# Kernel optimization log

Measured on AMD Instinct MI355X. Metric: run time of the kernel, lower is better.

## Reference

```python
import jax, jax.numpy as jnp
import numpy as np

HEAD_NUM = 8
QKV_DIM = 16
SQRT_EMBEDDING_DIM = 11.313708498984761  # sqrt(128)
LOGIT_CLIPPING = 10.0


def _reshape_by_heads(x):
    # x: [B, n, H*D] -> [B, H, n, D]
    B, n, _ = x.shape
    return x.reshape(B, n, HEAD_NUM, QKV_DIM).transpose(0, 2, 1, 3)


def setup_inputs() -> dict:
    key = jax.random.key(0)
    ks = jax.random.split(key, 12)
    B, P, N, E = 64, 500, 501, 128
    HD = HEAD_NUM * QKV_DIM
    s = 0.05
    return {
        "encoded_last_node": jax.random.normal(ks[0], (B, P, E), jnp.float32),
        "load": jax.random.uniform(ks[1], (B, P), jnp.float32),
        "ninf_mask": jnp.zeros((B, P, N), jnp.float32),
        "encoded_nodes": jax.random.normal(ks[2], (B, N, E), jnp.float32),
        "Wq_last": jax.random.normal(ks[3], (E + 1, HD), jnp.float32) * s,
        "Wk": jax.random.normal(ks[4], (E, HD), jnp.float32) * s,
        "Wv": jax.random.normal(ks[5], (E, HD), jnp.float32) * s,
        "mhc_W": jax.random.normal(ks[6], (HD, E), jnp.float32) * s,
        "mhc_b": jax.random.normal(ks[7], (E,), jnp.float32) * s,
        "new": jax.random.normal(ks[8], (B, HD, HD), jnp.float32) * s,
        "new_bias": jax.random.normal(ks[9], (B, 1, HD), jnp.float32) * s,
        "new_2": jax.random.normal(ks[10], (B, HD, HD), jnp.float32) * s,
        "new_bias_2": jax.random.normal(ks[11], (B, 1, HD), jnp.float32) * s,
    }


def reference(encoded_last_node, load, ninf_mask, encoded_nodes,
              Wq_last, Wk, Wv, mhc_W, mhc_b,
              new, new_bias, new_2, new_bias_2):
    B, P, E = encoded_last_node.shape
    # set_kv
    k = _reshape_by_heads(encoded_nodes @ Wk)            # [B,H,N,D]
    v = _reshape_by_heads(encoded_nodes @ Wv)            # [B,H,N,D]
    single_head_key = encoded_nodes.transpose(0, 2, 1)   # [B,E,N]

    # q from (last node embedding, load)
    input_cat = jnp.concatenate([encoded_last_node, load[:, :, None]], axis=2)  # [B,P,E+1]
    q = _reshape_by_heads(input_cat @ Wq_last)           # [B,H,P,D]

    # multi-head attention
    score = jnp.einsum('bhpd,bhnd->bhpn', q, k) / jnp.sqrt(jnp.float32(QKV_DIM))
    score = score + ninf_mask[:, None, :, :]
    attn = jax.nn.softmax(score, axis=3)
    out = jnp.einsum('bhpn,bhnd->bhpd', attn, v)         # [B,H,P,D]
    out_concat = out.transpose(0, 2, 1, 3).reshape(B, P, HEAD_NUM * QKV_DIM)

    # per-batch affine + relu + residual
    residual = out_concat
    h = jax.nn.relu(jnp.matmul(out_concat, new) + new_bias)
    h = jnp.matmul(h, new_2) + new_bias_2 + residual

    mh_atten_out = h @ mhc_W + mhc_b                     # [B,P,E]

    score2 = jnp.matmul(mh_atten_out, single_head_key)   # [B,P,N]
    score_clipped = LOGIT_CLIPPING * jnp.tanh(score2 / SQRT_EMBEDDING_DIM)
    probs = jax.nn.softmax(score_clipped + ninf_mask, axis=2)
    return probs
```

## Files before the change

### kernel.cpp

```cpp
#include <hip/hip_runtime.h>
#include <hip/hip_bf16.h>
#include <math.h>

typedef float f4 __attribute__((ext_vector_type(4)));

#define FMA __builtin_fmaf

#define BATCH 64
#define PP 500
#define NN 501

__global__ __launch_bounds__(256) void k_proj(
    const float* __restrict__ Xq,
    const float* __restrict__ Ld,
    const float* __restrict__ Xn,
    const float* __restrict__ Wq,
    const float* __restrict__ Wk, const float* __restrict__ Wv,
    float* __restrict__ Q, float* __restrict__ K_, float* __restrict__ V_)
{
  __shared__ float xs[64*132];
  const int t = threadIdx.x;
  const int tr = t >> 5, tc = t & 31;
  if (blockIdx.x < 500) {
    const int r0 = blockIdx.x * 64;
    for (int i = t; i < 64*32; i += 256) {
      int r = i >> 5, k4 = (i & 31) << 2;
      *(f4*)(xs + r*132 + k4) = *(const f4*)(Xq + (size_t)(r0+r)*128 + k4);
    }
    if (t < 64) xs[t*132 + 128] = Ld[r0 + t];
    __syncthreads();
    float acc[8][4];
    #pragma unroll
    for (int i = 0; i < 8; i++)
      #pragma unroll
      for (int c = 0; c < 4; c++) acc[i][c] = 0.f;
    for (int k4 = 0; k4 < 128; k4 += 4) {
      f4 x[8], w[4];
      #pragma unroll
      for (int j = 0; j < 4; j++) w[j] = *(const f4*)(Wq + (size_t)(k4+j)*128 + tc*4);
      #pragma unroll
      for (int i = 0; i < 8; i++) x[i] = *(const f4*)(xs + (tr*8+i)*132 + k4);
      #pragma unroll
      for (int i = 0; i < 8; i++)
        #pragma unroll
        for (int j = 0; j < 4; j++)
          #pragma unroll
          for (int c = 0; c < 4; c++)
            acc[i][c] = FMA(x[i][j], w[j][c], acc[i][c]);
    }
    {
      f4 w = *(const f4*)(Wq + (size_t)128*128 + tc*4);
      #pragma unroll
      for (int i = 0; i < 8; i++) {
        float xv = xs[(tr*8+i)*132 + 128];
        #pragma unroll
        for (int c = 0; c < 4; c++) acc[i][c] = FMA(xv, w[c], acc[i][c]);
      }
    }
    #pragma unroll
    for (int i = 0; i < 8; i++) {
      f4 o;
      #pragma unroll
      for (int c = 0; c < 4; c++) o[c] = acc[i][c];
      *(f4*)(Q + (size_t)(r0 + tr*8 + i)*128 + tc*4) = o;
    }
  } else {
    const int r0 = (blockIdx.x - 500) * 64;
    for (int i = t; i < 64*32; i += 256) {
      int r = i >> 5, k4 = (i & 31) << 2;
      *(f4*)(xs + r*132 + k4) = *(const f4*)(Xn + (size_t)(r0+r)*128 + k4);
    }
    __syncthreads();
    float accK[8][4], accV[8][4];
    #pragma unroll
    for (int i = 0; i < 8; i++)
      #pragma unroll
      for (int c = 0; c < 4; c++) { accK[i][c] = 0.f; accV[i][c] = 0.f; }
    for (int k4 = 0; k4 < 128; k4 += 4) {
      f4 x[8], wk[4], wv[4];
      #pragma unroll
      for (int j = 0; j < 4; j++) {
        wk[j] = *(const f4*)(Wk + (size_t)(k4+j)*128 + tc*4);
        wv[j] = *(const f4*)(Wv + (size_t)(k4+j)*128 + tc*4);
      }
      #pragma unroll
      for (int i = 0; i < 8; i++) x[i] = *(const f4*)(xs + (tr*8+i)*132 + k4);
      #pragma unroll
      for (int i = 0; i < 8; i++)
        #pragma unroll
        for (int j = 0; j < 4; j++)
          #pragma unroll
          for (int c = 0; c < 4; c++) {
            accK[i][c] = FMA(x[i][j], wk[j][c], accK[i][c]);
            accV[i][c] = FMA(x[i][j], wv[j][c], accV[i][c]);
          }
    }
    #pragma unroll
    for (int i = 0; i < 8; i++) {
      f4 ok, ov;
      #pragma unroll
      for (int c = 0; c < 4; c++) { ok[c] = accK[i][c]; ov[c] = accV[i][c]; }
      *(f4*)(K_ + (size_t)(r0 + tr*8 + i)*128 + tc*4) = ok;
      *(f4*)(V_ + (size_t)(r0 + tr*8 + i)*128 + tc*4) = ov;
    }
  }
}

__global__ __launch_bounds__(256, 4) void k_attn(
    const float* __restrict__ Q, const float* __restrict__ K_, const float* __restrict__ V_,
    const float* __restrict__ Msk, float* __restrict__ OC)
{
  __shared__ float ks[32*132];
  __shared__ float vs[32*132];
  __shared__ float mks[32*33];
  const int blk = blockIdx.x;
  const int b  = blk >> 4;
  const int pt = blk & 15;
  const int p0 = pt * 32;
  const int t = threadIdx.x;
  const int h   = t >> 5;
  const int row = t & 31;
  const bool pvalid = (p0 + row) < PP;
  const int p = pvalid ? (p0 + row) : (PP - 1);

  f4 q0, q1, q2, q3;
  {
    const float* qrow = Q + ((size_t)b*PP + p)*128 + h*16;
    q0 = *(const f4*)(qrow);
    q1 = *(const f4*)(qrow + 4);
    q2 = *(const f4*)(qrow + 8);
    q3 = *(const f4*)(qrow + 12);
  }

  const int mr = t >> 3, nq = (t & 7) << 2;
  const int grow = min(p0 + mr, PP - 1);
  const float* gm = Msk + ((size_t)b*PP + grow)*NN;

  float m_r = -1e30f, l_r = 0.f;
  f4 o0 = {0.f,0.f,0.f,0.f}, o1 = o0, o2 = o0, o3 = o0;

  f4 kpre[4], vpre[4]; float mk[4];
  #pragma unroll
  for (int u = 0; u < 4; u++) {
    int i = t + u*256;
    int n = i >> 5, d4 = (i & 31) << 2;
    kpre[u] = *(const f4*)(K_ + ((size_t)b*NN + n)*128 + d4);
    vpre[u] = *(const f4*)(V_ + ((size_t)b*NN + n)*128 + d4);
  }
  #pragma unroll
  for (int j = 0; j < 4; j++)
    mk[j] = (nq + j < NN) ? gm[nq + j] : -1e30f;

  for (int c0 = 0; c0 < NN; c0 += 32) {
    #pragma unroll
    for (int u = 0; u < 4; u++) {
      int i = t + u*256;
      int n = i >> 5, d4 = (i & 31) << 2;
      *(f4*)(ks + n*132 + d4) = kpre[u];
      *(f4*)(vs + n*132 + d4) = vpre[u];
    }
    {
      float* dm = mks + mr*33 + nq;
      #pragma unroll
      for (int j = 0; j < 4; j++) dm[j] = mk[j];
    }
    __syncthreads();

    const int c1 = c0 + 32;
    if (c1 < NN) {
      #pragma unroll
      for (int u = 0; u < 4; u++) {
        int i = t + u*256;
        int n = i >> 5, d4 = (i & 31) << 2;
        int ng = c1 + n;
        f4 kv = {0.f,0.f,0.f,0.f}, vv = {0.f,0.f,0.f,0.f};
        if (ng < NN) {
          kv = *(const f4*)(K_ + ((size_t)b*NN + ng)*128 + d4);
          vv = *(const f4*)(V_ + ((size_t)b*NN + ng)*128 + d4);
        }
        kpre[u] = kv; vpre[u] = vv;
      }
      #pragma unroll
      for (int j = 0; j < 4; j++)
        mk[j] = (c1 + nq + j < NN) ? gm[c1 + nq + j] : -1e30f;
    }

    const float* ksh = ks + h*16;
    const float* vsh = vs + h*16;
    const float* mrw = mks + row*33;
    #pragma unroll
    for (int n = 0; n < 32; n++) {
      const float* kf = ksh + n*132;
      f4 k0 = *(const f4*)(kf);
      f4 k1 = *(const f4*)(kf + 4);
      f4 k2 = *(const f4*)(kf + 8);
      f4 k3 = *(const f4*)(kf + 12);
      float s = 0.f;
      #pragma unroll
      for (int d = 0; d < 4; d++) s = FMA(q0[d], k0[d], s);
      #pragma unroll
      for (int d = 0; d < 4; d++) s = FMA(q1[d], k1[d], s);
      #pragma unroll
      for (int d = 0; d < 4; d++) s = FMA(q2[d], k2[d], s);
      #pragma unroll
      for (int d = 0; d < 4; d++) s = FMA(q3[d], k3[d], s);
      s = FMA(s, 0.25f, mrw[n]);
      if (s > m_r) {
        float cc = __expf(m_r - s);
        m_r = s;
        l_r *= cc;
        o0 *= cc; o1 *= cc; o2 *= cc; o3 *= cc;
      }
      float e = __expf(s - m_r);
      l_r += e;
      const float* vf = vsh + n*132;
      f4 v0 = *(const f4*)(vf);
      f4 v1 = *(const f4*)(vf + 4);
      f4 v2 = *(const f4*)(vf + 8);
      f4 v3 = *(const f4*)(vf + 12);
      #pragma unroll
      for (int d = 0; d < 4; d++) {
        o0[d] = FMA(e, v0[d], o0[d]);
        o1[d] = FMA(e, v1[d], o1[d]);
        o2[d] = FMA(e, v2[d], o2[d]);
        o3[d] = FMA(e, v3[d], o3[d]);
      }
    }
    __syncthreads();
  }

  if (pvalid) {
    float inv = 1.f / l_r;
    float* orow = OC + ((size_t)b*PP + p)*128 + h*16;
    *(f4*)(orow)      = o0 * inv;
    *(f4*)(orow + 4)  = o1 * inv;
    *(f4*)(orow + 8)  = o2 * inv;
    *(f4*)(orow + 12) = o3 * inv;
  }
}

__global__ __launch_bounds__(256) void k_ffn(
    const float* __restrict__ OC, const float* __restrict__ Wn, const float* __restrict__ Bn,
    const float* __restrict__ Wn2, const float* __restrict__ Bn2,
    const float* __restrict__ Wm, const float* __restrict__ Bm,
    float* __restrict__ MH)
{
  __shared__ float xs[64*132];
  __shared__ float hs[64*132];
  const int blk = blockIdx.x; const int b = blk >> 3, rb = blk & 7;
  const int r0 = rb*64;
  const int nv = min(64, PP - r0);
  const int t = threadIdx.x;
  const int tr = t >> 5, tc = t & 31;
  const float* ocb = OC + (size_t)b*PP*128;
  for (int i = t; i < 64*32; i += 256) {
    int r = i >> 5, k4 = (i & 31) << 2;
    f4 v = {0.f,0.f,0.f,0.f};
    if (r < nv) v = *(const f4*)(ocb + (size_t)(r0+r)*128 + k4);
    *(f4*)(xs + r*132 + k4) = v;
  }
  __syncthreads();
  {
    const float* W1 = Wn + (size_t)b*16384;
    float acc[8][4];
    #pragma unroll
    for (int i = 0; i < 8; i++)
      #pragma unroll
      for (int c = 0; c < 4; c++) acc[i][c] = 0.f;
    for (int k4 = 0; k4 < 128; k4 += 4) {
      f4 x[8], w[4];
      #pragma unroll
      for (int j = 0; j < 4; j++) w[j] = *(const f4*)(W1 + (size_t)(k4+j)*128 + tc*4);
      #pragma unroll
      for (int i = 0; i < 8; i++) x[i] = *(const f4*)(xs + (tr*8+i)*132 + k4);
      #pragma unroll
      for (int i = 0; i < 8; i++)
        #pragma unroll
        for (int j = 0; j < 4; j++)
          #pragma unroll
          for (int c = 0; c < 4; c++)
            acc[i][c] = FMA(x[i][j], w[j][c], acc[i][c]);
    }
    f4 b1 = *(const f4*)(Bn + b*128 + tc*4);
    #pragma unroll
    for (int i = 0; i < 8; i++) {
      f4 o;
      #pragma unroll
      for (int c = 0; c < 4; c++) o[c] = fmaxf(acc[i][c] + b1[c], 0.f);
      *(f4*)(hs + (tr*8+i)*132 + tc*4) = o;
    }
  }
  __syncthreads();
  float h2[8][4];
  {
    const float* W2 = Wn2 + (size_t)b*16384;
    float acc[8][4];
    #pragma unroll
    for (int i = 0; i < 8; i++)
      #pragma unroll
      for (int c = 0; c < 4; c++) acc[i][c] = 0.f;
    for (int k4 = 0; k4 < 128; k4 += 4) {
      f4 x[8], w[4];
      #pragma unroll
      for (int j = 0; j < 4; j++) w[j] = *(const f4*)(W2 + (size_t)(k4+j)*128 + tc*4);
      #pragma unroll
      for (int i = 0; i < 8; i++) x[i] = *(const f4*)(hs + (tr*8+i)*132 + k4);
      #pragma unroll
      for (int i = 0; i < 8; i++)
        #pragma unroll
        for (int j = 0; j < 4; j++)
          #pragma unroll
          for (int c = 0; c < 4; c++)
            acc[i][c] = FMA(x[i][j], w[j][c], acc[i][c]);
    }
    f4 b2 = *(const f4*)(Bn2 + b*128 + tc*4);
    #pragma unroll
    for (int i = 0; i < 8; i++)
      #pragma unroll
      for (int c = 0; c < 4; c++)
        h2[i][c] = acc[i][c] + b2[c] + xs[(tr*8+i)*132 + tc*4 + c];
  }
  __syncthreads();
  #pragma unroll
  for (int i = 0; i < 8; i++) {
    f4 o;
    #pragma unroll
    for (int c = 0; c < 4; c++) o[c] = h2[i][c];
    *(f4*)(hs + (tr*8+i)*132 + tc*4) = o;
  }
  __syncthreads();
  {
    float acc[8][4];
    #pragma unroll
    for (int i = 0; i < 8; i++)
      #pragma unroll
      for (int c = 0; c < 4; c++) acc[i][c] = 0.f;
    for (int k4 = 0; k4 < 128; k4 += 4) {
      f4 x[8], w[4];
      #pragma unroll
      for (int j = 0; j < 4; j++) w[j] = *(const f4*)(Wm + (size_t)(k4+j)*128 + tc*4);
      #pragma unroll
      for (int i = 0; i < 8; i++) x[i] = *(const f4*)(hs + (tr*8+i)*132 + k4);
      #pragma unroll
      for (int i = 0; i < 8; i++)
        #pragma unroll
        for (int j = 0; j < 4; j++)
          #pragma unroll
          for (int c = 0; c < 4; c++)
            acc[i][c] = FMA(x[i][j], w[j][c], acc[i][c]);
    }
    f4 b3 = *(const f4*)(Bm + tc*4);
    #pragma unroll
    for (int i = 0; i < 8; i++) {
      if (tr*8 + i < nv) {
        f4 o;
        #pragma unroll
        for (int c = 0; c < 4; c++) o[c] = acc[i][c] + b3[c];
        *(f4*)(MH + ((size_t)b*PP + r0 + tr*8 + i)*128 + tc*4) = o;
      }
    }
  }
}

__global__ __launch_bounds__(256, 3) void k_final(
    const float* __restrict__ MH, const float* __restrict__ EN,
    const float* __restrict__ Msk, float* __restrict__ OUT)
{
  __shared__ float ms[32*132];
  __shared__ float es[64*132];
  const int blk = blockIdx.x; const int b = blk >> 4, rb = blk & 15;
  const int r0 = rb*32; const int nv = min(32, PP - r0);
  const int t = threadIdx.x;
  const int tr = t >> 5, tc = t & 31;
  const float* mhb = MH + (size_t)(b*PP + r0)*128;
  for (int i = t; i < 32*32; i += 256) {
    int r = i >> 5, k4 = (i & 31) << 2;
    f4 v = {0.f,0.f,0.f,0.f};
    if (r < nv) v = *(const f4*)(mhb + (size_t)r*128 + k4);
    *(f4*)(ms + r*132 + k4) = v;
  }
  const float* enb = EN + (size_t)b*NN*128;
  f4 epre[8];
  #pragma unroll
  for (int u = 0; u < 8; u++) {
    int i = t + u*256;
    int n = i >> 5, k4 = (i & 31) << 2;
    f4 v = {0.f,0.f,0.f,0.f};
    if (n < NN) v = *(const f4*)(enb + (size_t)n*128 + k4);
    epre[u] = v;
  }
  float s[8][4][2];
  #pragma unroll
  for (int nt = 0; nt < 8; nt++) {
    #pragma unroll
    for (int u = 0; u < 8; u++) {
      int i = t + u*256;
      int n = i >> 5, k4 = (i & 31) << 2;
      *(f4*)(es + n*132 + k4) = epre[u];
    }
    __syncthreads();
    if (nt < 7) {
      const int n1 = (nt+1)*64;
      #pragma unroll
      for (int u = 0; u < 8; u++) {
        int i = t + u*256;
        int n = i >> 5, k4 = (i & 31) << 2;
        f4 v = {0.f,0.f,0.f,0.f};
        if (n1 + n < NN) v = *(const f4*)(enb + (size_t)(n1+n)*128 + k4);
        epre[u] = v;
      }
    }
    float acc[4][2];
    #pragma unroll
    for (int i = 0; i < 4; i++) { acc[i][0] = 0.f; acc[i][1] = 0.f; }
    #pragma unroll 8
    for (int k4 = 0; k4 < 128; k4 += 4) {
      f4 x[4];
      #pragma unroll
      for (int i = 0; i < 4; i++) x[i] = *(const f4*)(ms + (tr*4+i)*132 + k4);
      f4 e0 = *(const f4*)(es + tc*132 + k4);
      f4 e1 = *(const f4*)(es + (tc+32)*132 + k4);
      #pragma unroll
      for (int i = 0; i < 4; i++)
        #pragma unroll
        for (int j = 0; j < 4; j++) {
          acc[i][0] = FMA(x[i][j], e0[j], acc[i][0]);
          acc[i][1] = FMA(x[i][j], e1[j], acc[i][1]);
        }
    }
    #pragma unroll
    for (int i = 0; i < 4; i++) {
      s[nt][i][0] = acc[i][0];
      s[nt][i][1] = acc[i][1];
    }
    __syncthreads();
  }
  const float* mkb = Msk + (size_t)(b*PP + r0)*NN;
  #pragma unroll
  for (int nt = 0; nt < 8; nt++)
    #pragma unroll
    for (int i = 0; i < 4; i++)
      #pragma unroll
      for (int c = 0; c < 2; c++) {
        int r = tr*4 + i, n = nt*64 + tc + c*32;
        float val = -INFINITY;
        if (r < nv && n < NN) {
          float E = __expf(s[nt][i][c] * 0.17677669529663687f);
          val = 10.f - 20.f/(E + 1.f) + mkb[(size_t)r*NN + n];
        }
        s[nt][i][c] = val;
      }
  float* ob = OUT + (size_t)(b*PP + r0)*NN;
  #pragma unroll
  for (int i = 0; i < 4; i++) {
    float m = -INFINITY;
    #pragma unroll
    for (int nt = 0; nt < 8; nt++)
      #pragma unroll
      for (int c = 0; c < 2; c++) m = fmaxf(m, s[nt][i][c]);
    #pragma unroll
    for (int o = 16; o > 0; o >>= 1) m = fmaxf(m, __shfl_xor(m, o, 32));
    float l = 0.f;
    #pragma unroll
    for (int nt = 0; nt < 8; nt++)
      #pragma unroll
      for (int c = 0; c < 2; c++) {
        float e_ = __expf(s[nt][i][c] - m);
        s[nt][i][c] = e_;
        l += e_;
      }
    #pragma unroll
    for (int o = 16; o > 0; o >>= 1) l += __shfl_xor(l, o, 32);
    const int r = tr*4 + i;
    if (r < nv) {
      float inv = 1.f / l;
      float* orow = ob + (size_t)r*NN;
      #pragma unroll
      for (int nt = 0; nt < 8; nt++)
        #pragma unroll
        for (int c = 0; c < 2; c++) {
          int n = nt*64 + tc + c*32;
          if (n < NN) orow[n] = s[nt][i][c] * inv;
        }
    }
  }
}

extern "C" void kernel_launch(void* const* d_in, const int* in_sizes, int n_in,
                              void* d_out, int out_size, void* d_ws, size_t ws_size,
                              hipStream_t stream) {
  const float* eln  = (const float*)d_in[0];
  const float* load = (const float*)d_in[1];
  const float* mask = (const float*)d_in[2];
  const float* en   = (const float*)d_in[3];
  const float* Wq   = (const float*)d_in[4];
  const float* Wk   = (const float*)d_in[5];
  const float* Wv   = (const float*)d_in[6];
  const float* Wm   = (const float*)d_in[7];
  const float* Bm   = (const float*)d_in[8];
  const float* Wn   = (const float*)d_in[9];
  const float* Bn   = (const float*)d_in[10];
  const float* Wn2  = (const float*)d_in[11];
  const float* Bn2  = (const float*)d_in[12];
  float* out = (float*)d_out;
  float* ws  = (float*)d_ws;
  float* Q   = ws;
  float* K_  = ws + 4096000;
  float* V_  = ws + 8200192;
  float* OC  = ws + 12304384;
  float* MH  = ws + 16400384;
  hipLaunchKernelGGL(k_proj,  dim3(1001), dim3(256), 0, stream, eln, load, en, Wq, Wk, Wv, Q, K_, V_);
  hipLaunchKernelGGL(k_attn,  dim3(1024), dim3(256), 0, stream, Q, K_, V_, mask, OC);
  hipLaunchKernelGGL(k_ffn,   dim3(512),  dim3(256), 0, stream, OC, Wn, Bn, Wn2, Bn2, Wm, Bm, MH);
  hipLaunchKernelGGL(k_final, dim3(1024), dim3(256), 0, stream, MH, en, mask, out);
}
```

Measured before the change: 406.2 us.

## Fuse attention, FFN, projection and final softmax into one kernel

Merges k_attn, k_ffn and k_final into a single kernel that works on a 32-row tile per block. The attention output, the FFN intermediates and the mh output stay in shared memory instead of making round trips through global workspace, and two kernel launches go away. In exchange, the FFN tile shrinks from 64 to 32 rows, so per-batch weights are reloaded twice as often. The final score loop now uses 32-column tiles with a 16x4 register array. Occupancy is lowered to 3 blocks per SM, and the serial chain inside each block gets longer.

```diff
diff --git a/kernel.cpp b/kernel.cpp
--- a/kernel.cpp
+++ b/kernel.cpp
@@ -11,10 +11,8 @@
 #define NN 501
 
 __global__ __launch_bounds__(256) void k_proj(
-    const float* __restrict__ Xq,
-    const float* __restrict__ Ld,
-    const float* __restrict__ Xn,
-    const float* __restrict__ Wq,
+    const float* __restrict__ Xq, const float* __restrict__ Ld,
+    const float* __restrict__ Xn, const float* __restrict__ Wq,
     const float* __restrict__ Wk, const float* __restrict__ Wv,
     float* __restrict__ Q, float* __restrict__ K_, float* __restrict__ V_)
 {
@@ -106,382 +104,338 @@
   }
 }
 
-__global__ __launch_bounds__(256, 4) void k_attn(
+__global__ __launch_bounds__(256, 3) void k_fused(
     const float* __restrict__ Q, const float* __restrict__ K_, const float* __restrict__ V_,
-    const float* __restrict__ Msk, float* __restrict__ OC)
+    const float* __restrict__ Msk, const float* __restrict__ EN,
+    const float* __restrict__ Wn, const float* __restrict__ Bn,
+    const float* __restrict__ Wn2, const float* __restrict__ Bn2,
+    const float* __restrict__ Wm, const float* __restrict__ Bm,
+    float* __restrict__ OUT)
 {
-  __shared__ float ks[32*132];
-  __shared__ float vs[32*132];
+  __shared__ float sA[32*132];
+  __shared__ float sB[32*132];
   __shared__ float mks[32*33];
   const int blk = blockIdx.x;
   const int b  = blk >> 4;
   const int pt = blk & 15;
   const int p0 = pt * 32;
+  const int nv = min(32, PP - p0);
   const int t = threadIdx.x;
-  const int h   = t >> 5;
-  const int row = t & 31;
-  const bool pvalid = (p0 + row) < PP;
-  const int p = pvalid ? (p0 + row) : (PP - 1);
-
-  f4 q0, q1, q2, q3;
+
   {
-    const float* qrow = Q + ((size_t)b*PP + p)*128 + h*16;
-    q0 = *(const f4*)(qrow);
-    q1 = *(const f4*)(qrow + 4);
-    q2 = *(const f4*)(qrow + 8);
-    q3 = *(const f4*)(qrow + 12);
-  }
-
-  const int mr = t >> 3, nq = (t & 7) << 2;
-  const int grow = min(p0 + mr, PP - 1);
-  const float* gm = Msk + ((size_t)b*PP + grow)*NN;
-
-  float m_r = -1e30f, l_r = 0.f;
-  f4 o0 = {0.f,0.f,0.f,0.f}, o1 = o0, o2 = o0, o3 = o0;
-
-  f4 kpre[4], vpre[4]; float mk[4];
-  #pragma unroll
-  for (int u = 0; u < 4; u++) {
-    int i = t + u*256;
-    int n = i >> 5, d4 = (i & 31) << 2;
-    kpre[u] = *(const f4*)(K_ + ((size_t)b*NN + n)*128 + d4);
-    vpre[u] = *(const f4*)(V_ + ((size_t)b*NN + n)*128 + d4);
-  }
-  #pragma unroll
-  for (int j = 0; j < 4; j++)
-    mk[j] = (nq + j < NN) ? gm[nq + j] : -1e30f;
-
-  for (int c0 = 0; c0 < NN; c0 += 32) {
+    const int h   = t >> 5;
+    const int row = t & 31;
+    const bool pvalid = (p0 + row) < PP;
+    const int p = pvalid ? (p0 + row) : (PP - 1);
+
+    f4 q0, q1, q2, q3;
+    {
+      const float* qrow = Q + ((size_t)b*PP + p)*128 + h*16;
+      q0 = *(const f4*)(qrow);
+      q1 = *(const f4*)(qrow + 4);
+      q2 = *(const f4*)(qrow + 8);
+      q3 = *(const f4*)(qrow + 12);
+    }
+    const int mr = t >> 3, nq = (t & 7) << 2;
+    const int grow = min(p0 + mr, PP - 1);
+    const float* gm = Msk + ((size_t)b*PP + grow)*NN;
+
+    float m_r = -1e30f, l_r = 0.f;
+    f4 o0 = {0.f,0.f,0.f,0.f}, o1 = o0, o2 = o0, o3 = o0;
+
+    f4 kpre[4], vpre[4]; float mk[4];
     #pragma unroll
     for (int u = 0; u < 4; u++) {
       int i = t + u*256;
       int n = i >> 5, d4 = (i & 31) << 2;
-      *(f4*)(ks + n*132 + d4) = kpre[u];
-      *(f4*)(vs + n*132 + d4) = vpre[u];
-    }
-    {
-      float* dm = mks + mr*33 + nq;
-      #pragma unroll
-      for (int j = 0; j < 4; j++) dm[j] = mk[j];
-    }
-    __syncthreads();
-
-    const int c1 = c0 + 32;
-    if (c1 < NN) {
+      kpre[u] = *(const f4*)(K_ + ((size_t)b*NN + n)*128 + d4);
+      vpre[u] = *(const f4*)(V_ + ((size_t)b*NN + n)*128 + d4);
+    }
+    #pragma unroll
+    for (int j = 0; j < 4; j++)
+      mk[j] = (nq + j < NN) ? gm[nq + j] : -1e30f;
+
+    for (int c0 = 0; c0 < NN; c0 += 32) {
       #pragma unroll
       for (int u = 0; u < 4; u++) {
         int i = t + u*256;
         int n = i >> 5, d4 = (i & 31) << 2;
-        int ng = c1 + n;
-        f4 kv = {0.f,0.f,0.f,0.f}, vv = {0.f,0.f,0.f,0.f};
-        if (ng < NN) {
-          kv = *(const f4*)(K_ + ((size_t)b*NN + ng)*128 + d4);
-          vv = *(const f4*)(V_ + ((size_t)b*NN + ng)*128 + d4);
-        }
-        kpre[u] = kv; vpre[u] = vv;
-      }
-      #pragma unroll
-      for (int j = 0; j < 4; j++)
-        mk[j] = (c1 + nq + j < NN) ? gm[c1 + nq + j] : -1e30f;
-    }
-
-    const float* ksh = ks + h*16;
-    const float* vsh = vs + h*16;
-    const float* mrw = mks + row*33;
-    #pragma unroll
-    for (int n = 0; n < 32; n++) {
-      const float* kf = ksh + n*132;
-      f4 k0 = *(const f4*)(kf);
-      f4 k1 = *(const f4*)(kf + 4);
-      f4 k2 = *(const f4*)(kf + 8);
-      f4 k3 = *(const f4*)(kf + 12);
-      float s = 0.f;
-      #pragma unroll
-      for (int d = 0; d < 4; d++) s = FMA(q0[d], k0[d], s);
-      #pragma unroll
-      for (int d = 0; d < 4; d++) s = FMA(q1[d], k1[d], s);
-      #pragma unroll
-      for (int d = 0; d < 4; d++) s = FMA(q2[d], k2[d], s);
-      #pragma unroll
-      for (int d = 0; d < 4; d++) s = FMA(q3[d], k3[d], s);
-      s = FMA(s, 0.25f, mrw[n]);
-      if (s > m_r) {
-        float cc = __expf(m_r - s);
-        m_r = s;
-        l_r *= cc;
-        o0 *= cc; o1 *= cc; o2 *= cc; o3 *= cc;
-      }
-      float e = __expf(s - m_r);
-      l_r += e;
-      const float* vf = vsh + n*132;
-      f4 v0 = *(const f4*)(vf);
-      f4 v1 = *(const f4*)(vf + 4);
-      f4 v2 = *(const f4*)(vf + 8);
-      f4 v3 = *(const f4*)(vf + 12);
-      #pragma unroll
-      for (int d = 0; d < 4; d++) {
-        o0[d] = FMA(e, v0[d], o0[d]);
-        o1[d] = FMA(e, v1[d], o1[d]);
-        o2[d] = FMA(e, v2[d], o2[d]);
-        o3[d] = FMA(e, v3[d], o3[d]);
-      }
-    }
-    __syncthreads();
-  }
-
-  if (pvalid) {
+        *(f4*)(sA + n*132 + d4) = kpre[u];
+        *(f4*)(sB + n*132 + d4) = vpre[u];
+      }
+      {
+        float* dm = mks + mr*33 + nq;
+        #pragma unroll
+        for (int j = 0; j < 4; j++) dm[j] = mk[j];
+      }
+      __syncthreads();
+
+      const int c1 = c0 + 32;
+      if (c1 < NN) {
+        #pragma unroll
+        for (int u = 0; u < 4; u++) {
+          int i = t + u*256;
+          int n = i >> 5, d4 = (i & 31) << 2;
+          int ng = c1 + n;
+          f4 kv = {0.f,0.f,0.f,0.f}, vv = {0.f,0.f,0.f,0.f};
+          if (ng < NN) {
+            kv = *(const f4*)(K_ + ((size_t)b*NN + ng)*128 + d4);
+            vv = *(const f4*)(V_ + ((size_t)b*NN + ng)*128 + d4);
+          }
+          kpre[u] = kv; vpre[u] = vv;
+        }
+        #pragma unroll
+        for (int j = 0; j < 4; j++)
+          mk[j] = (c1 + nq + j < NN) ? gm[c1 + nq + j] : -1e30f;
+      }
+
+      const float* ksh = sA + h*16;
+      const float* vsh = sB + h*16;
+      const float* mrw = mks + row*33;
+      #pragma unroll
+      for (int n = 0; n < 32; n++) {
+        const float* kf = ksh + n*132;
+        f4 k0 = *(const f4*)(kf);
+        f4 k1 = *(const f4*)(kf + 4);
+        f4 k2 = *(const f4*)(kf + 8);
+        f4 k3 = *(const f4*)(kf + 12);
+        float s = 0.f;
+        #pragma unroll
+        for (int d = 0; d < 4; d++) s = FMA(q0[d], k0[d], s);
+        #pragma unroll
+        for (int d = 0; d < 4; d++) s = FMA(q1[d], k1[d], s);
+        #pragma unroll
+        for (int d = 0; d < 4; d++) s = FMA(q2[d], k2[d], s);
+        #pragma unroll
+        for (int d = 0; d < 4; d++) s = FMA(q3[d], k3[d], s);
+        s = FMA(s, 0.25f, mrw[n]);
+        if (s > m_r) {
+          float cc = __expf(m_r - s);
+          m_r = s;
+          l_r *= cc;
+          o0 *= cc; o1 *= cc; o2 *= cc; o3 *= cc;
+        }
+        float e = __expf(s - m_r);
+        l_r += e;
+        const float* vf = vsh + n*132;
+        f4 v0 = *(const f4*)(vf);
+        f4 v1 = *(const f4*)(vf + 4);
+        f4 v2 = *(const f4*)(vf + 8);
+        f4 v3 = *(const f4*)(vf + 12);
+        #pragma unroll
+        for (int d = 0; d < 4; d++) {
+          o0[d] = FMA(e, v0[d], o0[d]);
+          o1[d] = FMA(e, v1[d], o1[d]);
+          o2[d] = FMA(e, v2[d], o2[d]);
+          o3[d] = FMA(e, v3[d], o3[d]);
+        }
+      }
+      __syncthreads();
+    }
+
     float inv = 1.f / l_r;
-    float* orow = OC + ((size_t)b*PP + p)*128 + h*16;
-    *(f4*)(orow)      = o0 * inv;
-    *(f4*)(orow + 4)  = o1 * inv;
-    *(f4*)(orow + 8)  = o2 * inv;
-    *(f4*)(orow + 12) = o3 * inv;
-  }
-}
-
-__global__ __launch_bounds__(256) void k_ffn(
-    const float* __restrict__ OC, const float* __restrict__ Wn, const float* __restrict__ Bn,
-    const float* __restrict__ Wn2, const float* __restrict__ Bn2,
-    const float* __restrict__ Wm, const float* __restrict__ Bm,
-    float* __restrict__ MH)
-{
-  __shared__ float xs[64*132];
-  __shared__ float hs[64*132];
-  const int blk = blockIdx.x; const int b = blk >> 3, rb = blk & 7;
-  const int r0 = rb*64;
-  const int nv = min(64, PP - r0);
-  const int t = threadIdx.x;
-  const int tr = t >> 5, tc = t & 31;
-  const float* ocb = OC + (size_t)b*PP*128;
-  for (int i = t; i < 64*32; i += 256) {
-    int r = i >> 5, k4 = (i & 31) << 2;
-    f4 v = {0.f,0.f,0.f,0.f};
-    if (r < nv) v = *(const f4*)(ocb + (size_t)(r0+r)*128 + k4);
-    *(f4*)(xs + r*132 + k4) = v;
+    float* xr = sA + row*132 + h*16;
+    *(f4*)(xr)      = o0 * inv;
+    *(f4*)(xr + 4)  = o1 * inv;
+    *(f4*)(xr + 8)  = o2 * inv;
+    *(f4*)(xr + 12) = o3 * inv;
   }
   __syncthreads();
+
+  const int tr = t >> 5, tc = t & 31;
   {
-    const float* W1 = Wn + (size_t)b*16384;
-    float acc[8][4];
-    #pragma unroll
-    for (int i = 0; i < 8; i++)
-      #pragma unroll
-      for (int c = 0; c < 4; c++) acc[i][c] = 0.f;
-    for (int k4 = 0; k4 < 128; k4 += 4) {
-      f4 x[8], w[4];
-      #pragma unroll
-      for (int j = 0; j < 4; j++) w[j] = *(const f4*)(W1 + (size_t)(k4+j)*128 + tc*4);
-      #pragma unroll
-      for (int i = 0; i < 8; i++) x[i] = *(const f4*)(xs + (tr*8+i)*132 + k4);
-      #pragma unroll
-      for (int i = 0; i < 8; i++)
-        #pragma unroll
-        for (int j = 0; j < 4; j++)
-          #pragma unroll
-          for (int c = 0; c < 4; c++)
-            acc[i][c] = FMA(x[i][j], w[j][c], acc[i][c]);
-    }
-    f4 b1 = *(const f4*)(Bn + b*128 + tc*4);
-    #pragma unroll
-    for (int i = 0; i < 8; i++) {
+    {
+      const float* W1 = Wn + (size_t)b*16384;
+      float acc[4][4];
+      #pragma unroll
+      for (int i = 0; i < 4; i++)
+        #pragma unroll
+        for (int c = 0; c < 4; c++) acc[i][c] = 0.f;
+      for (int k4 = 0; k4 < 128; k4 += 4) {
+        f4 x[4], w[4];
+        #pragma unroll
+        for (int j = 0; j < 4; j++) w[j] = *(const f4*)(W1 + (size_t)(k4+j)*128 + tc*4);
+        #pragma unroll
+        for (int i = 0; i < 4; i++) x[i] = *(const f4*)(sA + (tr*4+i)*132 + k4);
+        #pragma unroll
+        for (int i = 0; i < 4; i++)
+          #pragma unroll
+          for (int j = 0; j < 4; j++)
+            #pragma unroll
+            for (int c = 0; c < 4; c++)
+              acc[i][c] = FMA(x[i][j], w[j][c], acc[i][c]);
+      }
+      f4 b1 = *(const f4*)(Bn + b*128 + tc*4);
+      #pragma unroll
+      for (int i = 0; i < 4; i++) {
+        f4 o;
+        #pragma unroll
+        for (int c = 0; c < 4; c++) o[c] = fmaxf(acc[i][c] + b1[c], 0.f);
+        *(f4*)(sB + (tr*4+i)*132 + tc*4) = o;
+      }
+    }
+    __syncthreads();
+    float h2[4][4];
+    {
+      const float* W2 = Wn2 + (size_t)b*16384;
+      float acc[4][4];
+      #pragma unroll
+      for (int i = 0; i < 4; i++)
+        #pragma unroll
+        for (int c = 0; c < 4; c++) acc[i][c] = 0.f;
+      for (int k4 = 0; k4 < 128; k4 += 4) {
+        f4 x[4], w[4];
+        #pragma unroll
+        for (int j = 0; j < 4; j++) w[j] = *(const f4*)(W2 + (size_t)(k4+j)*128 + tc*4);
+        #pragma unroll
+        for (int i = 0; i < 4; i++) x[i] = *(const f4*)(sB + (tr*4+i)*132 + k4);
+        #pragma unroll
+        for (int i = 0; i < 4; i++)
+          #pragma unroll
+          for (int j = 0; j < 4; j++)
+            #pragma unroll
+            for (int c = 0; c < 4; c++)
+              acc[i][c] = FMA(x[i][j], w[j][c], acc[i][c]);
+      }
+      f4 b2 = *(const f4*)(Bn2 + b*128 + tc*4);
+      #pragma unroll
+      for (int i = 0; i < 4; i++)
+        #pragma unroll
+        for (int c = 0; c < 4; c++)
+          h2[i][c] = acc[i][c] + b2[c] + sA[(tr*4+i)*132 + tc*4 + c];
+    }
+    __syncthreads();
+    #pragma unroll
+    for (int i = 0; i < 4; i++) {
       f4 o;
       #pragma unroll
-      for (int c = 0; c < 4; c++) o[c] = fmaxf(acc[i][c] + b1[c], 0.f);
-      *(f4*)(hs + (tr*8+i)*132 + tc*4) = o;
+      for (int c = 0; c < 4; c++) o[c] = h2[i][c];
+      *(f4*)(sB + (tr*4+i)*132 + tc*4) = o;
+    }
+    __syncthreads();
+    {
+      float acc[4][4];
+      #pragma unroll
+      for (int i = 0; i < 4; i++)
+        #pragma unroll
+        for (int c = 0; c < 4; c++) acc[i][c] = 0.f;
+      for (int k4 = 0; k4 < 128; k4 += 4) {
+        f4 x[4], w[4];
+        #pragma unroll
+        for (int j = 0; j < 4; j++) w[j] = *(const f4*)(Wm + (size_t)(k4+j)*128 + tc*4);
+        #pragma unroll
+        for (int i = 0; i < 4; i++) x[i] = *(const f4*)(sB + (tr*4+i)*132 + k4);
+        #pragma unroll
+        for (int i = 0; i < 4; i++)
+          #pragma unroll
+          for (int j = 0; j < 4; j++)
+            #pragma unroll
+            for (int c = 0; c < 4; c++)
+              acc[i][c] = FMA(x[i][j], w[j][c], acc[i][c]);
+      }
+      f4 b3 = *(const f4*)(Bm + tc*4);
+      #pragma unroll
+      for (int i = 0; i < 4; i++) {
+        f4 o;
+        #pragma unroll
+        for (int c = 0; c < 4; c++) o[c] = acc[i][c] + b3[c];
+        *(f4*)(sA + (tr*4+i)*132 + tc*4) = o;
+      }
     }
   }
   __syncthreads();
-  float h2[8][4];
+
   {
-    const float* W2 = Wn2 + (size_t)b*16384;
-    float acc[8][4];
-    #pragma unroll
-    for (int i = 0; i < 8; i++)
-      #pragma unroll
-      for (int c = 0; c < 4; c++) acc[i][c] = 0.f;
-    for (int k4 = 0; k4 < 128; k4 += 4) {
-      f4 x[8], w[4];
-      #pragma unroll
-      for (int j = 0; j < 4; j++) w[j] = *(const f4*)(W2 + (size_t)(k4+j)*128 + tc*4);
-      #pragma unroll
-      for (int i = 0; i < 8; i++) x[i] = *(const f4*)(hs + (tr*8+i)*132 + k4);
-      #pragma unroll
-      for (int i = 0; i < 8; i++)
-        #pragma unroll
-        for (int j = 0; j < 4; j++)
-          #pragma unroll
-          for (int c = 0; c < 4; c++)
-            acc[i][c] = FMA(x[i][j], w[j][c], acc[i][c]);
-    }
-    f4 b2 = *(const f4*)(Bn2 + b*128 + tc*4);
-    #pragma unroll
-    for (int i = 0; i < 8; i++)
-      #pragma unroll
-      for (int c = 0; c < 4; c++)
-        h2[i][c] = acc[i][c] + b2[c] + xs[(tr*8+i)*132 + tc*4 + c];
-  }
-  __syncthreads();
-  #pragma unroll
-  for (int i = 0; i < 8; i++) {
-    f4 o;
-    #pragma unroll
-    for (int c = 0; c < 4; c++) o[c] = h2[i][c];
-    *(f4*)(hs + (tr*8+i)*132 + tc*4) = o;
-  }
-  __syncthreads();
-  {
-    float acc[8][4];
-    #pragma unroll
-    for (int i = 0; i < 8; i++)
-      #pragma unroll
-      for (int c = 0; c < 4; c++) acc[i][c] = 0.f;
-    for (int k4 = 0; k4 < 128; k4 += 4) {
-      f4 x[8], w[4];
-      #pragma unroll
-      for (int j = 0; j < 4; j++) w[j] = *(const f4*)(Wm + (size_t)(k4+j)*128 + tc*4);
-      #pragma unroll
-      for (int i = 0; i < 8; i++) x[i] = *(const f4*)(hs + (tr*8+i)*132 + k4);
-      #pragma unroll
-      for (int i = 0; i < 8; i++)
-        #pragma unroll
-        for (int j = 0; j < 4; j++)
-          #pragma unroll
-          for (int c = 0; c < 4; c++)
-            acc[i][c] = FMA(x[i][j], w[j][c], acc[i][c]);
-    }
-    f4 b3 = *(const f4*)(Bm + tc*4);
-    #pragma unroll
-    for (int i = 0; i < 8; i++) {
-      if (tr*8 + i < nv) {
-        f4 o;
-        #pragma unroll
-        for (int c = 0; c < 4; c++) o[c] = acc[i][c] + b3[c];
-        *(f4*)(MH + ((size_t)b*PP + r0 + tr*8 + i)*128 + tc*4) = o;
-      }
-    }
-  }
-}
-
-__global__ __launch_bounds__(256, 3) void k_final(
-    const float* __restrict__ MH, const float* __restrict__ EN,
-    const float* __restrict__ Msk, float* __restrict__ OUT)
-{
-  __shared__ float ms[32*132];
-  __shared__ float es[64*132];
-  const int blk = blockIdx.x; const int b = blk >> 4, rb = blk & 15;
-  const int r0 = rb*32; const int nv = min(32, PP - r0);
-  const int t = threadIdx.x;
-  const int tr = t >> 5, tc = t & 31;
-  const float* mhb = MH + (size_t)(b*PP + r0)*128;
-  for (int i = t; i < 32*32; i += 256) {
-    int r = i >> 5, k4 = (i & 31) << 2;
-    f4 v = {0.f,0.f,0.f,0.f};
-    if (r < nv) v = *(const f4*)(mhb + (size_t)r*128 + k4);
-    *(f4*)(ms + r*132 + k4) = v;
-  }
-  const float* enb = EN + (size_t)b*NN*128;
-  f4 epre[8];
-  #pragma unroll
-  for (int u = 0; u < 8; u++) {
-    int i = t + u*256;
-    int n = i >> 5, k4 = (i & 31) << 2;
-    f4 v = {0.f,0.f,0.f,0.f};
-    if (n < NN) v = *(const f4*)(enb + (size_t)n*128 + k4);
-    epre[u] = v;
-  }
-  float s[8][4][2];
-  #pragma unroll
-  for (int nt = 0; nt < 8; nt++) {
-    #pragma unroll
-    for (int u = 0; u < 8; u++) {
+    const float* enb = EN + (size_t)b*NN*128;
+    f4 epre[4];
+    #pragma unroll
+    for (int u = 0; u < 4; u++) {
       int i = t + u*256;
       int n = i >> 5, k4 = (i & 31) << 2;
-      *(f4*)(es + n*132 + k4) = epre[u];
-    }
-    __syncthreads();
-    if (nt < 7) {
-      const int n1 = (nt+1)*64;
-      #pragma unroll
-      for (int u = 0; u < 8; u++) {
+      f4 v = {0.f,0.f,0.f,0.f};
+      if (n < NN) v = *(const f4*)(enb + (size_t)n*128 + k4);
+      epre[u] = v;
+    }
+    float s[16][4];
+    #pragma unroll
+    for (int nt = 0; nt < 16; nt++) {
+      #pragma unroll
+      for (int u = 0; u < 4; u++) {
         int i = t + u*256;
         int n = i >> 5, k4 = (i & 31) << 2;
-        f4 v = {0.f,0.f,0.f,0.f};
-        if (n1 + n < NN) v = *(const f4*)(enb + (size_t)(n1+n)*128 + k4);
-        epre[u] = v;
-      }
-    }
-    float acc[4][2];
-    #pragma unroll
-    for (int i = 0; i < 4; i++) { acc[i][0] = 0.f; acc[i][1] = 0.f; }
-    #pragma unroll 8
-    for (int k4 = 0; k4 < 128; k4 += 4) {
-      f4 x[4];
-      #pragma unroll
-      for (int i = 0; i < 4; i++) x[i] = *(const f4*)(ms + (tr*4+i)*132 + k4);
-      f4 e0 = *(const f4*)(es + tc*132 + k4);
-      f4 e1 = *(const f4*)(es + (tc+32)*132 + k4);
-      #pragma unroll
-      for (int i = 0; i < 4; i++)
-        #pragma unroll
-        for (int j = 0; j < 4; j++) {
-          acc[i][0] = FMA(x[i][j], e0[j], acc[i][0]);
-          acc[i][1] = FMA(x[i][j], e1[j], acc[i][1]);
-        }
-    }
-    #pragma unroll
-    for (int i = 0; i < 4; i++) {
-      s[nt][i][0] = acc[i][0];
-      s[nt][i][1] = acc[i][1];
-    }
-    __syncthreads();
-  }
-  const float* mkb = Msk + (size_t)(b*PP + r0)*NN;
-  #pragma unroll
-  for (int nt = 0; nt < 8; nt++)
-    #pragma unroll
-    for (int i = 0; i < 4; i++)
-      #pragma unroll
-      for (int c = 0; c < 2; c++) {
-        int r = tr*4 + i, n = nt*64 + tc + c*32;
+        *(f4*)(sB + n*132 + k4) = epre[u];
+      }
+      __syncthreads();
+      if (nt < 15) {
+        const int n1 = (nt+1)*32;
+        #pragma unroll
+        for (int u = 0; u < 4; u++) {
+          int i = t + u*256;
+          int n = i >> 5, k4 = (i & 31) << 2;
+          f4 v = {0.f,0.f,0.f,0.f};
+          if (n1 + n < NN) v = *(const f4*)(enb + (size_t)(n1+n)*128 + k4);
+          epre[u] = v;
+        }
+      }
+      float acc[4];
+      #pragma unroll
+      for (int i = 0; i < 4; i++) acc[i] = 0.f;
+      #pragma unroll 8
+      for (int k4 = 0; k4 < 128; k4 += 4) {
+        f4 x[4];
+        #pragma unroll
+        for (int i = 0; i < 4; i++) x[i] = *(const f4*)(sA + (tr*4+i)*132 + k4);
+        f4 e0 = *(const f4*)(sB + tc*132 + k4);
+        #pragma unroll
+        for (int i = 0; i < 4; i++)
+          #pragma unroll
+          for (int j = 0; j < 4; j++)
+            acc[i] = FMA(x[i][j], e0[j], acc[i]);
+      }
+      #pragma unroll
+      for (int i = 0; i < 4; i++) s[nt][i] = acc[i];
+      __syncthreads();
+    }
+    const float* mkb = Msk + (size_t)(b*PP + p0)*NN;
+    #pragma unroll
+    for (int nt = 0; nt < 16; nt++)
+      #pragma unroll
+      for (int i = 0; i < 4; i++) {
+        int r = tr*4 + i, n = nt*32 + tc;
         float val = -INFINITY;
         if (r < nv && n < NN) {
-          float E = __expf(s[nt][i][c] * 0.17677669529663687f);
+          float E = __expf(s[nt][i] * 0.17677669529663687f);
           val = 10.f - 20.f/(E + 1.f) + mkb[(size_t)r*NN + n];
         }
-        s[nt][i][c] = val;
-      }
-  float* ob = OUT + (size_t)(b*PP + r0)*NN;
-  #pragma unroll
-  for (int i = 0; i < 4; i++) {
-    float m = -INFINITY;
-    #pragma unroll
-    for (int nt = 0; nt < 8; nt++)
-      #pragma unroll
-      for (int c = 0; c < 2; c++) m = fmaxf(m, s[nt][i][c]);
-    #pragma unroll
-    for (int o = 16; o > 0; o >>= 1) m = fmaxf(m, __shfl_xor(m, o, 32));
-    float l = 0.f;
-    #pragma unroll
-    for (int nt = 0; nt < 8; nt++)
-      #pragma unroll
-      for (int c = 0; c < 2; c++) {
-        float e_ = __expf(s[nt][i][c] - m);
-        s[nt][i][c] = e_;
+        s[nt][i] = val;
+      }
+    float* ob = OUT + (size_t)(b*PP + p0)*NN;
+    #pragma unroll
+    for (int i = 0; i < 4; i++) {
+      float m = -INFINITY;
+      #pragma unroll
+      for (int nt = 0; nt < 16; nt++) m = fmaxf(m, s[nt][i]);
+      #pragma unroll
+      for (int o = 16; o > 0; o >>= 1) m = fmaxf(m, __shfl_xor(m, o, 32));
+      float l = 0.f;
+      #pragma unroll
+      for (int nt = 0; nt < 16; nt++) {
+        float e_ = __expf(s[nt][i] - m);
+        s[nt][i] = e_;
         l += e_;
       }
-    #pragma unroll
-    for (int o = 16; o > 0; o >>= 1) l += __shfl_xor(l, o, 32);
-    const int r = tr*4 + i;
-    if (r < nv) {
-      float inv = 1.f / l;
-      float* orow = ob + (size_t)r*NN;
-      #pragma unroll
-      for (int nt = 0; nt < 8; nt++)
-        #pragma unroll
-        for (int c = 0; c < 2; c++) {
-          int n = nt*64 + tc + c*32;
-          if (n < NN) orow[n] = s[nt][i][c] * inv;
-        }
+      #pragma unroll
+      for (int o = 16; o > 0; o >>= 1) l += __shfl_xor(l, o, 32);
+      const int r = tr*4 + i;
+      if (r < nv) {
+        float inv = 1.f / l;
+        float* orow = ob + (size_t)r*NN;
+        #pragma unroll
+        for (int nt = 0; nt < 16; nt++) {
+          int n = nt*32 + tc;
+          if (n < NN) orow[n] = s[nt][i] * inv;
+        }
+      }
     }
   }
 }
@@ -507,10 +461,7 @@
   float* Q   = ws;
   float* K_  = ws + 4096000;
   float* V_  = ws + 8200192;
-  float* OC  = ws + 12304384;
-  float* MH  = ws + 16400384;
   hipLaunchKernelGGL(k_proj,  dim3(1001), dim3(256), 0, stream, eln, load, en, Wq, Wk, Wv, Q, K_, V_);
-  hipLaunchKernelGGL(k_attn,  dim3(1024), dim3(256), 0, stream, Q, K_, V_, mask, OC);
-  hipLaunchKernelGGL(k_ffn,   dim3(512),  dim3(256), 0, stream, OC, Wn, Bn, Wn2, Bn2, Wm, Bm, MH);
-  hipLaunchKernelGGL(k_final, dim3(1024), dim3(256), 0, stream, MH, en, mask, out);
+  hipLaunchKernelGGL(k_fused, dim3(1024), dim3(256), 0, stream, Q, K_, V_, mask, en,
+                     Wn, Bn, Wn2, Bn2, Wm, Bm, out);
 }
```

Measured after the change: 440.1 us. 8.3% more time.
